# Performance work log

Measured on AMD Instinct MI355X. Metric: run time of the kernel, lower is better.

The kernel has to match this reference:

```python
import jax, jax.numpy as jnp
import numpy as np

N_STEPS = 2
MAX_STEP = 1.0
EPS64 = float(np.finfo(np.float64).eps)


def _sphere_log(p, q):
    # log map on unit sphere, tangent at p pointing to q; p,q: [..., D]
    cos = jnp.clip(jnp.sum(p * q, axis=-1, keepdims=True), -1.0, 1.0)
    u = q - cos * p
    un = jnp.linalg.norm(u, axis=-1, keepdims=True)
    theta = jnp.arccos(cos)
    return theta * u / (un + 1e-12)


def _sphere_exp(p, v):
    # exp map on unit sphere; jnp.sinc(n/pi) = sin(n)/n (stable at 0)
    n = jnp.linalg.norm(v, axis=-1, keepdims=True)
    x = jnp.cos(n) * p + jnp.sinc(n / jnp.pi) * v
    return x / jnp.linalg.norm(x, axis=-1, keepdims=True)


def setup_inputs() -> dict:
    key = jax.random.key(0)
    ks = jax.random.split(key, 6)
    N, C, D, E = 50000, 16, 3, 1600000
    nodes = jax.random.normal(ks[0], (N, C, D), dtype=jnp.float32)
    nodes = nodes / jnp.linalg.norm(nodes, axis=-1, keepdims=True)  # points on S^2
    edge_w = jax.random.uniform(ks[1], (E,), dtype=jnp.float32)
    senders = jax.random.randint(ks[2], (E,), 0, N, dtype=jnp.int32)
    receivers = jax.random.randint(ks[3], (E,), 0, N, dtype=jnp.int32)
    t_sqrt = 1.0 + 0.3 * jax.random.normal(ks[4], (C,), dtype=jnp.float32)
    delta_sqrt = 1.0 + 0.3 * jax.random.normal(ks[5], (C,), dtype=jnp.float32)
    return {"nodes": nodes, "edge_w": edge_w, "t_sqrt": t_sqrt,
            "delta_sqrt": delta_sqrt, "senders": senders, "receivers": receivers}


def reference(nodes, edge_w, t_sqrt, delta_sqrt, senders, receivers):
    N = nodes.shape[0]
    t = (t_sqrt ** 2) / N_STEPS            # per-channel time, split across Euler steps
    delta = delta_sqrt ** 2                 # per-channel min step size
    deg = jax.ops.segment_sum(edge_w, senders, num_segments=N)  # [N]

    def laplace(x):
        # graph Laplacian of manifold-valued signal: weighted mean of log maps, negated
        logs = _sphere_log(x[senders], x[receivers])              # [E, C, D]
        agg = jax.ops.segment_sum(edge_w[:, None, None] * logs, senders, num_segments=N)
        return -agg / (deg[:, None, None] + 1e-12)                # [N, C, D]

    def step(x, _):
        v = laplace(x)
        nrm = jnp.sqrt(jnp.sum(v * v, axis=-1) + EPS64)           # [N, C]
        alp = jax.nn.sigmoid(nrm - delta[None, :])
        scale = jnp.where(nrm * alp <= MAX_STEP, alp, MAX_STEP / nrm)
        v = -(v * scale[..., None]) * t[None, :, None]
        return _sphere_exp(x, v), None

    x, _ = jax.lax.scan(step, nodes, None, length=N_STEPS, unroll=N_STEPS)
    return x
```

## Files before the change

kernel.cpp:

```cpp
#include <hip/hip_runtime.h>
#include <math.h>


constexpr float EPS64F = 2.2204460492503131e-16f;
constexpr float PI_F   = 3.14159265358979323846f;
constexpr int   CH_BITS = 15;

typedef int      vi4 __attribute__((ext_vector_type(4)));
typedef float    vf4 __attribute__((ext_vector_type(4)));
typedef float    vf2 __attribute__((ext_vector_type(2)));
typedef _Float16 vh4 __attribute__((ext_vector_type(4)));


__global__ __launch_bounds__(1024) void lhist_kernel(
    const int* __restrict__ snd, unsigned char* __restrict__ pos,
    unsigned char* __restrict__ partial2, int E, int N) {
  extern __shared__ int h32[];
  int tid = threadIdx.x;
  int c = blockIdx.x;
  int nW = (N + 3) >> 2;
  for (int i = tid; i < nW; i += 1024) h32[i] = 0;
  __syncthreads();
  int base = c << CH_BITS;
  int cnt = min(1 << CH_BITS, E - base);
  const vi4* snd4 = (const vi4*)(snd + base);
  int cnt4 = cnt >> 2;
  for (int i = tid; i < cnt4; i += 1024) {
    vi4 sv = snd4[i];
    int e = base + (i << 2);
    int v, sh, old;
    v = sv.x; sh = (v & 3) << 3;
    old = atomicAdd(&h32[v >> 2], 1 << sh);
    pos[e]     = (unsigned char)((old >> sh) & 255);
    v = sv.y; sh = (v & 3) << 3;
    old = atomicAdd(&h32[v >> 2], 1 << sh);
    pos[e + 1] = (unsigned char)((old >> sh) & 255);
    v = sv.z; sh = (v & 3) << 3;
    old = atomicAdd(&h32[v >> 2], 1 << sh);
    pos[e + 2] = (unsigned char)((old >> sh) & 255);
    v = sv.w; sh = (v & 3) << 3;
    old = atomicAdd(&h32[v >> 2], 1 << sh);
    pos[e + 3] = (unsigned char)((old >> sh) & 255);
  }
  if (tid == 0) {
    for (int i = cnt4 << 2; i < cnt; ++i) {
      int v = snd[base + i];
      int sh = (v & 3) << 3;
      int old = atomicAdd(&h32[v >> 2], 1 << sh);
      pos[base + i] = (unsigned char)((old >> sh) & 255);
    }
  }
  __syncthreads();
  unsigned char* dst = partial2 + (size_t)c * N;
  const unsigned char* hb = (const unsigned char*)h32;
  for (int i = tid; i < N; i += 1024) dst[i] = hb[i];
}

__global__ __launch_bounds__(256) void scan1A_kernel(
    const unsigned char* __restrict__ partial2, unsigned char* __restrict__ boffL,
    int* __restrict__ row_start, int* __restrict__ btot,
    unsigned char* __restrict__ degU, int N, int NC) {
  __shared__ int wsum[4];
  int tid = threadIdx.x;
  int lane = tid & 63, wave = tid >> 6;
  int i = blockIdx.x * 256 + tid;
  int vpad = 0;
  if (i < N) {
    int run = 0;
    for (int c = 0; c < NC; ++c) {
      int t = partial2[(size_t)c * N + i];
      boffL[(size_t)c * N + i] = (unsigned char)run;
      run += t;
    }
    degU[i] = (unsigned char)run;
    vpad = (run + 7) & ~7;
  }
  int incl = vpad;
  #pragma unroll
  for (int off = 1; off < 64; off <<= 1) {
    int t = __shfl_up(incl, off, 64);
    if (lane >= off) incl += t;
  }
  if (lane == 63) wsum[wave] = incl;
  __syncthreads();
  if (wave == 0 && lane < 4) {
    int wincl = wsum[lane];
    #pragma unroll
    for (int off = 1; off < 4; off <<= 1) {
      int t = __shfl_up(wincl, off, 64);
      if (lane >= off) wincl += t;
    }
    wsum[lane] = wincl;
  }
  __syncthreads();
  int woff = (wave > 0) ? wsum[wave - 1] : 0;
  if (i < N) row_start[i] = woff + incl - vpad;
  if (tid == 0) btot[blockIdx.x] = wsum[3];
}

__global__ __launch_bounds__(256) void scanCD_kernel(
    int* __restrict__ row_start, const int* __restrict__ btot,
    const unsigned char* __restrict__ degU, int* __restrict__ pair,
    const float* __restrict__ nodes, vh4* __restrict__ nodes_h4,
    int N, int nb) {
  __shared__ int bsh[256];
  __shared__ int wtot[4];
  int tid = threadIdx.x;
  int lane = tid & 63, wave = tid >> 6;
  int v = (tid < nb) ? btot[tid] : 0;
  int incl = v;
  #pragma unroll
  for (int off = 1; off < 64; off <<= 1) {
    int t = __shfl_up(incl, off, 64);
    if (lane >= off) incl += t;
  }
  if (lane == 63) wtot[wave] = incl;
  __syncthreads();
  if (wave == 0 && lane < 4) {
    int wincl = wtot[lane];
    #pragma unroll
    for (int off = 1; off < 4; off <<= 1) {
      int t = __shfl_up(wincl, off, 64);
      if (lane >= off) wincl += t;
    }
    wtot[lane] = wincl;
  }
  __syncthreads();
  int woff = (wave > 0) ? wtot[wave - 1] : 0;
  bsh[tid] = woff + incl - v;
  if (blockIdx.x == 0 && tid == 0) row_start[N] = wtot[3];
  __syncthreads();
  int i = blockIdx.x * 256 + tid;
  if (i < N) {
    int rs = row_start[i] + bsh[blockIdx.x];
    row_start[i] = rs;
    int dg = degU[i];
    int pd = (dg + 7) & ~7;
    for (int j = rs + dg; j < rs + pd; ++j) pair[j] = 0;
  }
  int total = N * 16;
  for (int idx = blockIdx.x * 256 + tid; idx < total; idx += gridDim.x * 256) {
    const float* s = nodes + idx * 3;
    vh4 h = {(_Float16)s[0], (_Float16)s[1], (_Float16)s[2], (_Float16)0.f};
    nodes_h4[idx] = h;
  }
}

__global__ __launch_bounds__(256) void fill_kernel(
    const vi4* __restrict__ snd4, const vi4* __restrict__ rcv4,
    const vf4* __restrict__ ew4, const unsigned char* __restrict__ pos,
    const unsigned char* __restrict__ boffL, const int* __restrict__ row_start,
    int* __restrict__ pair,
    const int* __restrict__ snd, const int* __restrict__ rcv,
    const float* __restrict__ ew, int N, int E) {
  int tid = threadIdx.x;
  int E4 = E >> 2;
  #pragma unroll
  for (int gg = 0; gg < 2; ++gg) {
    int g = blockIdx.x * 512 + gg * 256 + tid;
    if (g < E4) {
      int e = g << 2;
      const unsigned char* bc = boffL + (size_t)(e >> CH_BITS) * N;
      vi4 s = __builtin_nontemporal_load(&snd4[g]);
      vi4 r = __builtin_nontemporal_load(&rcv4[g]);
      vf4 w = __builtin_nontemporal_load(&ew4[g]);
      unsigned pb = *(const unsigned*)(pos + e);
      int rs0 = row_start[s.x] + bc[s.x];
      int rs1 = row_start[s.y] + bc[s.y];
      int rs2 = row_start[s.z] + bc[s.z];
      int rs3 = row_start[s.w] + bc[s.w];
      unsigned e0 = ((unsigned)(int)fmaf(w.x, 65535.f, 0.5f) << 16) | (unsigned)r.x;
      unsigned e1 = ((unsigned)(int)fmaf(w.y, 65535.f, 0.5f) << 16) | (unsigned)r.y;
      unsigned e2 = ((unsigned)(int)fmaf(w.z, 65535.f, 0.5f) << 16) | (unsigned)r.z;
      unsigned e3 = ((unsigned)(int)fmaf(w.w, 65535.f, 0.5f) << 16) | (unsigned)r.w;
      pair[rs0 + (pb & 255u)]         = (int)e0;
      pair[rs1 + ((pb >> 8) & 255u)]  = (int)e1;
      pair[rs2 + ((pb >> 16) & 255u)] = (int)e2;
      pair[rs3 + (pb >> 24)]          = (int)e3;
    }
  }
  if (blockIdx.x == 0 && tid == 0) {
    for (int e = E4 << 2; e < E; ++e) {
      int sn = snd[e];
      pair[row_start[sn] + boffL[(size_t)(e >> CH_BITS) * N + sn] + pos[e]] =
          (int)(((unsigned)(int)fmaf(ew[e], 65535.f, 0.5f) << 16) | (unsigned)rcv[e]);
    }
  }
}


__device__ __forceinline__ void edge_accum_pk(
    vf2 p0, vf2 p1, vf2 p2, vf2 q0, vf2 q1, vf2 q2, vf2 w,
    vf2& a0, vf2& a1, vf2& a2) {
  vf2 cs = p0 * q0 + p1 * q1 + p2 * q2;
  cs = __builtin_elementwise_min(vf2{1.f, 1.f},
       __builtin_elementwise_max(vf2{-1.f, -1.f}, cs));
  vf2 u0 = q0 - cs * p0;
  vf2 u1 = q1 - cs * p1;
  vf2 u2 = q2 - cs * p2;
  vf2 un2 = __builtin_elementwise_max(u0 * u0 + u1 * u1 + u2 * u2,
                                      vf2{1e-24f, 1e-24f});
  vf2 ax = __builtin_elementwise_abs(cs);
  vf2 s = __builtin_elementwise_sqrt(vf2{1.f, 1.f} - ax);
  vf2 poly = ((ax * -0.0187293f + 0.0742610f) * ax - 0.2121144f) * ax
             + 1.5707288f;
  vf2 th = s * poly;
  vf2 theta;
  theta.x = (cs.x >= 0.0f) ? th.x : (PI_F - th.x);
  theta.y = (cs.y >= 0.0f) ? th.y : (PI_F - th.y);
  vf2 rsq;
  rsq.x = __builtin_amdgcn_rsqf(un2.x);
  rsq.y = __builtin_amdgcn_rsqf(un2.y);
  vf2 coef = w * theta * rsq;
  a0 += coef * u0;
  a1 += coef * u1;
  a2 += coef * u2;
}

__device__ __forceinline__ void node_step(
    float a0, float a1, float a2, float ws, float p0, float p1, float p2,
    float ts, float dsv, float& y0, float& y1, float& y2) {
  float invdg = __builtin_amdgcn_rcpf(ws + 1e-12f);
  float g0 = a0 * invdg, g1 = a1 * invdg, g2 = a2 * invdg;
  float nrm = sqrtf(fmaf(g0, g0, fmaf(g1, g1, g2 * g2)) + EPS64F);
  float tch = ts * ts * 0.5f;
  float dch = dsv * dsv;
  float alp = __builtin_amdgcn_rcpf(1.0f + __expf(dch - nrm));
  float scale = (nrm * alp <= 1.0f) ? alp : __builtin_amdgcn_rcpf(nrm);
  float f = scale * tch;
  float v0 = g0 * f, v1 = g1 * f, v2 = g2 * f;
  float nv = sqrtf(fmaf(v0, v0, fmaf(v1, v1, v2 * v2)));
  float cn = __cosf(nv);
  float sc = (nv > 1e-20f) ? (__sinf(nv) * __builtin_amdgcn_rcpf(nv)) : 1.0f;
  float t0 = fmaf(cn, p0, sc * v0);
  float t1 = fmaf(cn, p1, sc * v1);
  float t2 = fmaf(cn, p2, sc * v2);
  float inv = __builtin_amdgcn_rsqf(fmaf(t0, t0, fmaf(t1, t1, t2 * t2)));
  y0 = t0 * inv; y1 = t1 * inv; y2 = t2 * inv;
}

__global__ __launch_bounds__(256, 8) void flowp_kernel(
    const vh4* __restrict__ xh4, const float* __restrict__ pf,
    const int* __restrict__ row_start, const int* __restrict__ pair,
    const float* __restrict__ tsq, const float* __restrict__ dsq,
    float* __restrict__ of, vh4* __restrict__ oh4, int N) {
  int node = blockIdx.x * 4 + (threadIdx.x >> 6);
  if (node >= N) return;
  int lane = threadIdx.x & 63;
  int c = lane & 15;
  int k = lane >> 4;
  int c3 = c * 3;
  int beg = row_start[node];
  int end = row_start[node + 1];
  int ip = node * 48 + c3;
  float ps0 = pf[ip], ps1 = pf[ip + 1], ps2 = pf[ip + 2];
  vf2 p0 = {ps0, ps0}, p1 = {ps1, ps1}, p2 = {ps2, ps2};
  vf2 a0 = {0.f, 0.f}, a1 = {0.f, 0.f}, a2 = {0.f, 0.f}, wsv = {0.f, 0.f};
  const vh4* __restrict__ xc = xh4 + c;
  int iters = (end - beg) >> 3;
  int j = beg + k;
  constexpr float WS = 1.0f / 65535.0f;
  #pragma unroll 2
  for (int t = 0; t < iters; ++t, j += 8) {
    int e0 = pair[j];
    int e1 = pair[j + 4];
    float w0 = (float)((unsigned)e0 >> 16) * WS;
    float w1 = (float)((unsigned)e1 >> 16) * WS;
    vh4 qva = xc[(e0 & 0xFFFF) << 4];
    vh4 qvb = xc[(e1 & 0xFFFF) << 4];
    float qa0 = (float)qva.x, qa1 = (float)qva.y, qa2 = (float)qva.z;
    float qb0 = (float)qvb.x, qb1 = (float)qvb.y, qb2 = (float)qvb.z;
    vf2 wA = {w0, w1};
    edge_accum_pk(p0, p1, p2, vf2{qa0, qb0}, vf2{qa1, qb1},
                  vf2{qa2, qb2}, wA, a0, a1, a2);
    wsv += wA;
  }
  float A0 = a0.x + a0.y, A1 = a1.x + a1.y, A2 = a2.x + a2.y;
  float ws = wsv.x + wsv.y;
  A0 += __shfl_xor(A0, 16); A1 += __shfl_xor(A1, 16);
  A2 += __shfl_xor(A2, 16); ws += __shfl_xor(ws, 16);
  A0 += __shfl_xor(A0, 32); A1 += __shfl_xor(A1, 32);
  A2 += __shfl_xor(A2, 32); ws += __shfl_xor(ws, 32);
  if (k == 0) {
    float y0, y1, y2;
    node_step(A0, A1, A2, ws, ps0, ps1, ps2, tsq[c], dsq[c], y0, y1, y2);
    of[ip] = y0; of[ip + 1] = y1; of[ip + 2] = y2;
    if (oh4) {
      vh4 h = {(_Float16)y0, (_Float16)y1, (_Float16)y2, (_Float16)0.f};
      oh4[node * 16 + c] = h;
    }
  }
}

static inline size_t al16(size_t x) { return (x + 15) & ~(size_t)15; }

extern "C" void kernel_launch(void* const* d_in, const int* in_sizes, int n_in,
                              void* d_out, int out_size, void* d_ws, size_t ws_size,
                              hipStream_t stream) {
  const float* nodes = (const float*)d_in[0];
  const float* ew    = (const float*)d_in[1];
  const float* tsq   = (const float*)d_in[2];
  const float* dsq   = (const float*)d_in[3];
  const int*   snd   = (const int*)d_in[4];
  const int*   rcv   = (const int*)d_in[5];
  float* out = (float*)d_out;

  int E = in_sizes[1];
  int N = in_sizes[0] / 48;

  int NC = (E + (1 << CH_BITS) - 1) >> CH_BITS;

  size_t padN  = (size_t)E + 7 * (size_t)N + 64;
  size_t rsB   = al16((size_t)(N + 4) * 4);
  size_t auxB  = al16(1024 + (size_t)N + 64);
  size_t pairB = al16(padN * 4);
  size_t p2B   = al16((size_t)NC * N);
  size_t xh4B  = al16((size_t)N * 16 * 8);
  size_t boffB = al16((size_t)NC * N * 4);
  if (p2B + boffB < 2 * xh4B) boffB = 2 * xh4B - p2B;

  char* base = (char*)d_ws;
  int*           row_start = (int*)base;
  int*           btot      = (int*)(base + rsB);
  unsigned char* degU      = (unsigned char*)(base + rsB + 1024);
  int*           pair      = (int*)(base + rsB + auxB);
  unsigned char* partial2  = (unsigned char*)(base + rsB + auxB + pairB);
  unsigned char* boffL     = partial2 + p2B;
  unsigned char* pos       = boffL + boffB;
  vh4*           xtmp_h4   = (vh4*)partial2;
  vh4*           nodes_h4  = (vh4*)(partial2 + xh4B);

  int E4  = E >> 2;
  int nb  = (N + 255) / 256;
  int fbk = (E4 + 511) / 512;
  int nfb = (N + 3) / 4;
  size_t ldsB = (size_t)(((N + 3) >> 2)) * 4;

  lhist_kernel<<<NC, 1024, ldsB, stream>>>(snd, pos, partial2, E, N);
  scan1A_kernel<<<nb, 256, 0, stream>>>(partial2, boffL, row_start, btot,
                                        degU, N, NC);
  scanCD_kernel<<<nb, 256, 0, stream>>>(row_start, btot, degU, pair,
                                        nodes, nodes_h4, N, nb);
  fill_kernel<<<fbk, 256, 0, stream>>>((const vi4*)snd, (const vi4*)rcv,
                                       (const vf4*)ew, pos, boffL, row_start,
                                       pair, snd, rcv, ew, N, E);

  flowp_kernel<<<nfb, 256, 0, stream>>>(nodes_h4, nodes, row_start, pair,
                                        tsq, dsq, out, xtmp_h4, N);
  flowp_kernel<<<nfb, 256, 0, stream>>>(xtmp_h4, out, row_start, pair,
                                        tsq, dsq, out, nullptr, N);
}
```

Before: 250.1 us.

## Fuse block-offset scan into scan1A via last-block ticket, drop scanCD kernel

Removes the separate scanCD kernel launch by having the last-arriving block of scan1A (detected with an atomic ticket) compute the per-block exclusive prefix into bshG. Row starts are no longer globally fixed up; fill and flow kernels add bshG[node>>8] on the fly, and pair padding zeroing moves into fill_kernel. This saves one launch and a pass over row_start, at the cost of extra gathered loads of bshG in fill and flow kernels. Padding zeroing and pair writes now share a kernel with no ordering between them, but they target disjoint slots.

```diff
diff --git a/kernel.cpp b/kernel.cpp
--- a/kernel.cpp
+++ b/kernel.cpp
@@ -14,10 +14,12 @@
 
 __global__ __launch_bounds__(1024) void lhist_kernel(
     const int* __restrict__ snd, unsigned char* __restrict__ pos,
-    unsigned char* __restrict__ partial2, int E, int N) {
+    unsigned char* __restrict__ partial2, int* __restrict__ ticket,
+    int E, int N) {
   extern __shared__ int h32[];
   int tid = threadIdx.x;
   int c = blockIdx.x;
+  if (c == 0 && tid == 0) *ticket = 0;
   int nW = (N + 3) >> 2;
   for (int i = tid; i < nW; i += 1024) h32[i] = 0;
   __syncthreads();
@@ -59,8 +61,12 @@
 __global__ __launch_bounds__(256) void scan1A_kernel(
     const unsigned char* __restrict__ partial2, unsigned char* __restrict__ boffL,
     int* __restrict__ row_start, int* __restrict__ btot,
-    unsigned char* __restrict__ degU, int N, int NC) {
+    unsigned char* __restrict__ degU, int* __restrict__ ticket,
+    int* __restrict__ bshG, const float* __restrict__ nodes,
+    vh4* __restrict__ nodes_h4, int N, int NC, int nb) {
   __shared__ int wsum[4];
+  __shared__ int wtot[4];
+  __shared__ int lastFlag;
   int tid = threadIdx.x;
   int lane = tid & 63, wave = tid >> 6;
   int i = blockIdx.x * 256 + tid;
@@ -94,55 +100,41 @@
   }
   __syncthreads();
   int woff = (wave > 0) ? wsum[wave - 1] : 0;
-  if (i < N) row_start[i] = woff + incl - vpad;
+  if (i <= N) row_start[i] = woff + incl - vpad;
   if (tid == 0) btot[blockIdx.x] = wsum[3];
-}
-
-__global__ __launch_bounds__(256) void scanCD_kernel(
-    int* __restrict__ row_start, const int* __restrict__ btot,
-    const unsigned char* __restrict__ degU, int* __restrict__ pair,
-    const float* __restrict__ nodes, vh4* __restrict__ nodes_h4,
-    int N, int nb) {
-  __shared__ int bsh[256];
-  __shared__ int wtot[4];
-  int tid = threadIdx.x;
-  int lane = tid & 63, wave = tid >> 6;
-  int v = (tid < nb) ? btot[tid] : 0;
-  int incl = v;
-  #pragma unroll
-  for (int off = 1; off < 64; off <<= 1) {
-    int t = __shfl_up(incl, off, 64);
-    if (lane >= off) incl += t;
-  }
-  if (lane == 63) wtot[wave] = incl;
-  __syncthreads();
-  if (wave == 0 && lane < 4) {
-    int wincl = wtot[lane];
-    #pragma unroll
-    for (int off = 1; off < 4; off <<= 1) {
-      int t = __shfl_up(wincl, off, 64);
-      if (lane >= off) wincl += t;
-    }
-    wtot[lane] = wincl;
-  }
-  __syncthreads();
-  int woff = (wave > 0) ? wtot[wave - 1] : 0;
-  bsh[tid] = woff + incl - v;
-  if (blockIdx.x == 0 && tid == 0) row_start[N] = wtot[3];
-  __syncthreads();
-  int i = blockIdx.x * 256 + tid;
-  if (i < N) {
-    int rs = row_start[i] + bsh[blockIdx.x];
-    row_start[i] = rs;
-    int dg = degU[i];
-    int pd = (dg + 7) & ~7;
-    for (int j = rs + dg; j < rs + pd; ++j) pair[j] = 0;
-  }
   int total = N * 16;
-  for (int idx = blockIdx.x * 256 + tid; idx < total; idx += gridDim.x * 256) {
+  int nthr = gridDim.x * 256;
+  for (int idx = blockIdx.x * 256 + tid; idx < total; idx += nthr) {
     const float* s = nodes + idx * 3;
     vh4 h = {(_Float16)s[0], (_Float16)s[1], (_Float16)s[2], (_Float16)0.f};
     nodes_h4[idx] = h;
+  }
+  __threadfence();
+  if (tid == 0) lastFlag = (atomicAdd(ticket, 1) == (int)gridDim.x - 1);
+  __syncthreads();
+  if (lastFlag) {
+    __threadfence();
+    int v = (tid < nb) ? ((volatile int*)btot)[tid] : 0;
+    int ic = v;
+    #pragma unroll
+    for (int off = 1; off < 64; off <<= 1) {
+      int t = __shfl_up(ic, off, 64);
+      if (lane >= off) ic += t;
+    }
+    if (lane == 63) wtot[wave] = ic;
+    __syncthreads();
+    if (wave == 0 && lane < 4) {
+      int wincl = wtot[lane];
+      #pragma unroll
+      for (int off = 1; off < 4; off <<= 1) {
+        int t = __shfl_up(wincl, off, 64);
+        if (lane >= off) wincl += t;
+      }
+      wtot[lane] = wincl;
+    }
+    __syncthreads();
+    int wo = (wave > 0) ? wtot[wave - 1] : 0;
+    bshG[tid] = wo + ic - v;
   }
 }
 
@@ -150,11 +142,18 @@
     const vi4* __restrict__ snd4, const vi4* __restrict__ rcv4,
     const vf4* __restrict__ ew4, const unsigned char* __restrict__ pos,
     const unsigned char* __restrict__ boffL, const int* __restrict__ row_start,
+    const int* __restrict__ bshG, const unsigned char* __restrict__ degU,
     int* __restrict__ pair,
     const int* __restrict__ snd, const int* __restrict__ rcv,
     const float* __restrict__ ew, int N, int E) {
   int tid = threadIdx.x;
   int E4 = E >> 2;
+  for (int i = blockIdx.x * 256 + tid; i < N; i += gridDim.x * 256) {
+    int rs = row_start[i] + bshG[i >> 8];
+    int dg = degU[i];
+    int pd = (dg + 7) & ~7;
+    for (int j = rs + dg; j < rs + pd; ++j) pair[j] = 0;
+  }
   #pragma unroll
   for (int gg = 0; gg < 2; ++gg) {
     int g = blockIdx.x * 512 + gg * 256 + tid;
@@ -165,10 +164,10 @@
       vi4 r = __builtin_nontemporal_load(&rcv4[g]);
       vf4 w = __builtin_nontemporal_load(&ew4[g]);
       unsigned pb = *(const unsigned*)(pos + e);
-      int rs0 = row_start[s.x] + bc[s.x];
-      int rs1 = row_start[s.y] + bc[s.y];
-      int rs2 = row_start[s.z] + bc[s.z];
-      int rs3 = row_start[s.w] + bc[s.w];
+      int rs0 = row_start[s.x] + bshG[s.x >> 8] + bc[s.x];
+      int rs1 = row_start[s.y] + bshG[s.y >> 8] + bc[s.y];
+      int rs2 = row_start[s.z] + bshG[s.z >> 8] + bc[s.z];
+      int rs3 = row_start[s.w] + bshG[s.w >> 8] + bc[s.w];
       unsigned e0 = ((unsigned)(int)fmaf(w.x, 65535.f, 0.5f) << 16) | (unsigned)r.x;
       unsigned e1 = ((unsigned)(int)fmaf(w.y, 65535.f, 0.5f) << 16) | (unsigned)r.y;
       unsigned e2 = ((unsigned)(int)fmaf(w.z, 65535.f, 0.5f) << 16) | (unsigned)r.z;
@@ -182,7 +181,7 @@
   if (blockIdx.x == 0 && tid == 0) {
     for (int e = E4 << 2; e < E; ++e) {
       int sn = snd[e];
-      pair[row_start[sn] + boffL[(size_t)(e >> CH_BITS) * N + sn] + pos[e]] =
+      pair[row_start[sn] + bshG[sn >> 8] + boffL[(size_t)(e >> CH_BITS) * N + sn] + pos[e]] =
           (int)(((unsigned)(int)fmaf(ew[e], 65535.f, 0.5f) << 16) | (unsigned)rcv[e]);
     }
   }
@@ -241,17 +240,18 @@
 
 __global__ __launch_bounds__(256, 8) void flowp_kernel(
     const vh4* __restrict__ xh4, const float* __restrict__ pf,
-    const int* __restrict__ row_start, const int* __restrict__ pair,
-    const float* __restrict__ tsq, const float* __restrict__ dsq,
-    float* __restrict__ of, vh4* __restrict__ oh4, int N) {
+    const int* __restrict__ row_start, const int* __restrict__ bshG,
+    const int* __restrict__ pair, const float* __restrict__ tsq,
+    const float* __restrict__ dsq, float* __restrict__ of,
+    vh4* __restrict__ oh4, int N) {
   int node = blockIdx.x * 4 + (threadIdx.x >> 6);
   if (node >= N) return;
   int lane = threadIdx.x & 63;
   int c = lane & 15;
   int k = lane >> 4;
   int c3 = c * 3;
-  int beg = row_start[node];
-  int end = row_start[node + 1];
+  int beg = row_start[node] + bshG[node >> 8];
+  int end = row_start[node + 1] + bshG[(node + 1) >> 8];
   int ip = node * 48 + c3;
   float ps0 = pf[ip], ps1 = pf[ip + 1], ps2 = pf[ip + 2];
   vf2 p0 = {ps0, ps0}, p1 = {ps1, ps1}, p2 = {ps2, ps2};
@@ -312,7 +312,7 @@
 
   size_t padN  = (size_t)E + 7 * (size_t)N + 64;
   size_t rsB   = al16((size_t)(N + 4) * 4);
-  size_t auxB  = al16(1024 + (size_t)N + 64);
+  size_t auxB  = al16(2048 + 64 + (size_t)N);
   size_t pairB = al16(padN * 4);
   size_t p2B   = al16((size_t)NC * N);
   size_t xh4B  = al16((size_t)N * 16 * 8);
@@ -322,7 +322,9 @@
   char* base = (char*)d_ws;
   int*           row_start = (int*)base;
   int*           btot      = (int*)(base + rsB);
-  unsigned char* degU      = (unsigned char*)(base + rsB + 1024);
+  int*           bshG      = (int*)(base + rsB + 1024);
+  int*           ticket    = (int*)(base + rsB + 2048);
+  unsigned char* degU      = (unsigned char*)(base + rsB + 2048 + 64);
   int*           pair      = (int*)(base + rsB + auxB);
   unsigned char* partial2  = (unsigned char*)(base + rsB + auxB + pairB);
   unsigned char* boffL     = partial2 + p2B;
@@ -336,17 +338,16 @@
   int nfb = (N + 3) / 4;
   size_t ldsB = (size_t)(((N + 3) >> 2)) * 4;
 
-  lhist_kernel<<<NC, 1024, ldsB, stream>>>(snd, pos, partial2, E, N);
+  lhist_kernel<<<NC, 1024, ldsB, stream>>>(snd, pos, partial2, ticket, E, N);
   scan1A_kernel<<<nb, 256, 0, stream>>>(partial2, boffL, row_start, btot,
-                                        degU, N, NC);
-  scanCD_kernel<<<nb, 256, 0, stream>>>(row_start, btot, degU, pair,
-                                        nodes, nodes_h4, N, nb);
+                                        degU, ticket, bshG, nodes, nodes_h4,
+                                        N, NC, nb);
   fill_kernel<<<fbk, 256, 0, stream>>>((const vi4*)snd, (const vi4*)rcv,
                                        (const vf4*)ew, pos, boffL, row_start,
-                                       pair, snd, rcv, ew, N, E);
-
-  flowp_kernel<<<nfb, 256, 0, stream>>>(nodes_h4, nodes, row_start, pair,
-                                        tsq, dsq, out, xtmp_h4, N);
-  flowp_kernel<<<nfb, 256, 0, stream>>>(xtmp_h4, out, row_start, pair,
-                                        tsq, dsq, out, nullptr, N);
-}
+                                       bshG, degU, pair, snd, rcv, ew, N, E);
+
+  flowp_kernel<<<nfb, 256, 0, stream>>>(nodes_h4, nodes, row_start, bshG,
+                                        pair, tsq, dsq, out, xtmp_h4, N);
+  flowp_kernel<<<nfb, 256, 0, stream>>>(xtmp_h4, out, row_start, bshG,
+                                        pair, tsq, dsq, out, nullptr, N);
+}
```

Measured after the change: 267.4 us. 1.07x slower.
